# Performance work log

Hardware: AMD Instinct MI355X
Metric: run time of the kernel (lower is better)

## Reference

```python
import jax, jax.numpy as jnp
import numpy as np

G, K1, K2, N, NP, EPS = 16, 128, 32, 128, 512, 1e-5

def _bn(x, axes):
    m = jnp.mean(x, axes, keepdims=True)
    v = jnp.var(x, axes, keepdims=True)  # biased, as torch BN training mode
    return (x - m) * jax.lax.rsqrt(v + EPS)

def _fps(xyz, npoint):
    # farthest point sampling, deterministic start at index 0; xyz (B,P,3)
    B, P, _ = xyz.shape
    def step(carry, _):
        dists, far = carry
        c = jnp.take_along_axis(xyz, far[:, None, None], axis=1)   # (B,1,3)
        d = jnp.sum((xyz - c) ** 2, -1)                            # (B,P)
        dists = jnp.minimum(dists, d)
        return (dists, jnp.argmax(dists, -1)), far
    init = (jnp.full((B, P), 1e10, xyz.dtype), jnp.zeros((B,), jnp.int32))
    _, idx = jax.lax.scan(step, init, None, length=npoint)         # (npoint,B)
    return jnp.take_along_axis(xyz, idx.T[:, :, None], axis=1)     # (B,npoint,3)

def _pointnet(x, w1, b1, w2, b2, w3, b3):
    h = jax.nn.relu(_bn(x @ w1 + b1, (0, 1)))
    h = jax.nn.relu(_bn(h @ w2 + b2, (0, 1)))
    h = _bn(h @ w3 + b3, (0, 1))
    return jnp.max(h, axis=1)                                      # (B,1024)

def _mapping(feat, w1, b1, w2, b2, w3, b3, w4, b4):
    # all 16 branches stacked on leading axis g
    h = jax.nn.relu(_bn(jnp.einsum('bk,gkj->gbj', feat, w1) + b1[:, None, :], (1,)))
    h = jax.nn.relu(_bn(jnp.einsum('gbj,gjk->gbk', h, w2) + b2[:, None, :], (1,)))
    h = jax.nn.relu(_bn(jnp.einsum('gbj,gjk->gbk', h, w3) + b3[:, None, :], (1,)))
    return jax.nn.relu(_bn(jnp.einsum('gbj,gjk->gbk', h, w4) + b4[:, None, :], (1,)))

def _axform(feat, fw, fb, c1w, c1b, c2w, c2b, c3w, c3b, c4w, c4b):
    # feat (G,B,K1); 1x1 convs expressed as einsums in channels-last layout
    xb = (jnp.einsum('gbk,gkm->gbm', feat, fw) + fb[:, None, :]).reshape(G, -1, N, K2)
    h = jax.nn.relu(_bn(jnp.einsum('gbnk,gkc->gbnc', xb, c1w) + c1b[:, None, None, :], (1, 2)))
    h = jax.nn.relu(_bn(jnp.einsum('gbnc,gcd->gbnd', h, c2w) + c2b[:, None, None, :], (1, 2)))
    h = jnp.einsum('gbnd,gde->gbne', h, c3w) + c3b[:, None, None, :]  # (G,B,N,1024)
    w = jax.nn.softmax(h, axis=2)                                     # softmax over N
    y = jnp.einsum('gbne,gbnk->gbek', w, xb)                          # (G,B,1024,K2)
    return jnp.einsum('gbek,gkc->gbec', y, c4w) + c4b[:, None, None, :]  # (G,B,1024,3)

def _forward(x, pn, mp, gen, ref):
    x_partial = _fps(x, NP)                                           # (B,512,3)
    feat = _pointnet(x, *pn)                                          # (B,1024)
    mfeat = _mapping(feat, *mp)                                       # (G,B,K1)
    x1g = _axform(mfeat, *gen)                                        # (G,B,1024,3)
    B = x.shape[0]
    x_1 = jnp.transpose(x1g, (1, 0, 2, 3)).reshape(B, -1, 3)          # (B,16384,3)
    fps1 = jax.vmap(lambda p: _fps(p, NP))(x1g)                       # (G,B,512,3)
    x_base = jnp.concatenate([fps1, jnp.broadcast_to(x_partial, (G,) + x_partial.shape)], axis=2)
    x2g = x_base + _axform(mfeat, *ref)                               # (G,B,1024,3)
    x_2 = jnp.transpose(x2g, (1, 0, 2, 3)).reshape(B, -1, 3)
    return x_1, x_2

def setup_inputs() -> dict:
    keys = iter(jax.random.split(jax.random.key(0), 40))
    def rn(shape, s=0.02):
        return (s * jax.random.normal(next(keys), shape)).astype(jnp.float32)
    inp = {}
    inp['x'] = jax.random.normal(next(keys), (16, 2048, 3), jnp.float32)
    inp['pn_w1'] = rn((3, 64));      inp['pn_b1'] = rn((64,))
    inp['pn_w2'] = rn((64, 128));    inp['pn_b2'] = rn((128,))
    inp['pn_w3'] = rn((128, 1024));  inp['pn_b3'] = rn((1024,))
    inp['mp_w1'] = rn((G, 1024, 1024)); inp['mp_b1'] = rn((G, 1024))
    inp['mp_w2'] = rn((G, 1024, 1024)); inp['mp_b2'] = rn((G, 1024))
    inp['mp_w3'] = rn((G, 1024, 1024)); inp['mp_b3'] = rn((G, 1024))
    inp['mp_w4'] = rn((G, 1024, K1));   inp['mp_b4'] = rn((G, K1))
    for p in ('g', 'r'):
        inp[p + '_fw'] = rn((G, K1, N * K2)); inp[p + '_fb'] = rn((G, N * K2))
        inp[p + '_c1w'] = rn((G, K2, 64));    inp[p + '_c1b'] = rn((G, 64))
        inp[p + '_c2w'] = rn((G, 64, 128));   inp[p + '_c2b'] = rn((G, 128))
        inp[p + '_c3w'] = rn((G, 128, 1024)); inp[p + '_c3b'] = rn((G, 1024))
        inp[p + '_c4w'] = rn((G, K2, 3));     inp[p + '_c4b'] = rn((G, 3))
    return inp

def reference(x, pn_w1, pn_b1, pn_w2, pn_b2, pn_w3, pn_b3,
              mp_w1, mp_b1, mp_w2, mp_b2, mp_w3, mp_b3, mp_w4, mp_b4,
              g_fw, g_fb, g_c1w, g_c1b, g_c2w, g_c2b, g_c3w, g_c3b, g_c4w, g_c4b,
              r_fw, r_fb, r_c1w, r_c1b, r_c2w, r_c2b, r_c3w, r_c3b, r_c4w, r_c4b):
    pn = (pn_w1, pn_b1, pn_w2, pn_b2, pn_w3, pn_b3)
    mp = (mp_w1, mp_b1, mp_w2, mp_b2, mp_w3, mp_b3, mp_w4, mp_b4)
    gen = (g_fw, g_fb, g_c1w, g_c1b, g_c2w, g_c2b, g_c3w, g_c3b, g_c4w, g_c4b)
    ref = (r_fw, r_fb, r_c1w, r_c1b, r_c2w, r_c2b, r_c3w, r_c3b, r_c4w, r_c4b)
    return _forward(x, pn, mp, gen, ref)
```

## Files before the change

kernel.cpp:

```cpp
#include <hip/hip_runtime.h>
#include <math.h>

#define TID ((int)threadIdx.x)

namespace {
constexpr float EPSf = 1e-5f;

struct FpsArgs {
  const float* pts; float* out; float* dmin; int* far;
  int it0, it1, nc;
};

__device__ __forceinline__ unsigned fenc(float f){
  unsigned u = __float_as_uint(f);
  return (u & 0x80000000u) ? ~u : (u | 0x80000000u);
}
__device__ __forceinline__ float fdec(unsigned e){
  unsigned u = (e & 0x80000000u) ? (e & 0x7fffffffu) : ~e;
  return __uint_as_float(u);
}

template<int CTRL>
__device__ __forceinline__ void dpp_comb(float& bm, int& bp){
  int om_i = __builtin_amdgcn_update_dpp(__float_as_int(bm), __float_as_int(bm), CTRL, 0xf, 0xf, false);
  int op   = __builtin_amdgcn_update_dpp(bp, bp, CTRL, 0xf, 0xf, false);
  float om = __int_as_float(om_i);
  if (om > bm || (om == bm && op < bp)){ bm = om; bp = op; }
}

template<int LP, int NT>
__device__ void fps_body(const FpsArgs& a, int ci){
  const int NPTS = NT*LP;
  const float* pts = a.pts + (size_t)ci * NPTS * 3;
  float* out = a.out + (size_t)ci * 512 * 3;
  float* dst = a.dmin + (size_t)ci * NPTS;
  float px[LP], py[LP], pz[LP], dmin[LP];
#pragma unroll
  for (int j = 0; j < LP; j++){
    int p = TID + NT*j;
    px[j] = pts[p*3+0]; py[j] = pts[p*3+1]; pz[j] = pts[p*3+2];
  }
  int far;
  if (a.it0 == 0){
#pragma unroll
    for (int j = 0; j < LP; j++) dmin[j] = 1e10f;
    far = 0;
  } else {
#pragma unroll
    for (int j = 0; j < LP; j++) dmin[j] = dst[TID + NT*j];
    far = a.far[ci];
  }
  __shared__ unsigned long long red2[2][NT/64];
  for (int i = a.it0; i < a.it1; i++){
    float cx = pts[far*3+0], cy = pts[far*3+1], cz = pts[far*3+2];
    if (TID == 0){ out[i*3+0]=cx; out[i*3+1]=cy; out[i*3+2]=cz; }
    float bm = -1.f; int bp = 0;
#pragma unroll
    for (int j = 0; j < LP; j++){
      float dx = __fsub_rn(px[j], cx);
      float dy = __fsub_rn(py[j], cy);
      float dz = __fsub_rn(pz[j], cz);
      float d  = __fadd_rn(__fadd_rn(__fmul_rn(dx,dx), __fmul_rn(dy,dy)), __fmul_rn(dz,dz));
      float dm = fminf(dmin[j], d);
      dmin[j] = dm;
      if (dm > bm){ bm = dm; bp = TID + NT*j; }
    }
    dpp_comb<0x111>(bm,bp); dpp_comb<0x112>(bm,bp); dpp_comb<0x114>(bm,bp);
    dpp_comb<0x118>(bm,bp); dpp_comb<0x142>(bm,bp); dpp_comb<0x143>(bm,bp);
    unsigned long long key =
      ((unsigned long long)(unsigned)__builtin_amdgcn_readlane(__float_as_int(bm), 63) << 32)
      | (unsigned)~(unsigned)__builtin_amdgcn_readlane(bp, 63);
    if ((TID & 63) == 63) red2[i&1][TID>>6] = key;
    __syncthreads();
    unsigned long long kk = red2[i&1][0];
#pragma unroll
    for (int t = 1; t < NT/64; t++){
      unsigned long long o = red2[i&1][t];
      kk = kk > o ? kk : o;
    }
    far = (int)~(unsigned)kk;
  }
  if (a.it1 < 512){
#pragma unroll
    for (int j = 0; j < LP; j++) dst[TID + NT*j] = dmin[j];
    if (TID == 0) a.far[ci] = far;
  }
}

__device__ __forceinline__ int aswz64(int n, int k){
  return (n << 6) + ((((k >> 2) ^ ((n >> 3) & 3)) << 2) | (k & 3));
}
__device__ __forceinline__ int pswz(int n, int e){
  return (n << 6) + (e ^ (((n >> 3) & 3) << 3));
}

template<int C, int K, int FLP>
__global__ void __launch_bounds__(256) rowgemm_kernel(const float* __restrict__ in,
    const float* __restrict__ w, const float* __restrict__ bias, const float2* __restrict__ st2,
    float* __restrict__ out, int rows_per_g, FpsArgs fa)
{
  int bid = blockIdx.x;
  if constexpr (FLP > 0){
    if (bid < fa.nc){ fps_body<FLP,256>(fa, bid); return; }
    bid -= fa.nc;
  }
  constexpr int RPB = 256 / C;
  __shared__ float lin[RPB * K];
  size_t row0 = (size_t)bid * RPB;
  int g = (int)(row0 / rows_per_g);
  for (int i = TID; i < RPB*K; i += 256){
    float v = in[row0*(size_t)K + i];
    if (st2){ float2 s = st2[(size_t)g*K + (i % K)]; v = fmaxf((v - s.x)*s.y, 0.f); }
    lin[i] = v;
  }
  __syncthreads();
  int r = TID / C, c = TID % C;
  float acc = bias[(size_t)g*C + c];
  const float* wg = w + (size_t)g*K*C + c;
#pragma unroll
  for (int k = 0; k < K; k++) acc = fmaf(lin[r*K + k], wg[(size_t)k*C], acc);
  out[(row0 + r)*C + c] = acc;
}

template<int FLP>
__global__ void __launch_bounds__(256, 4) big1024b_kernel(const float* __restrict__ in,
    const float* __restrict__ w, const float* __restrict__ bias, const float2* __restrict__ st2,
    float* __restrict__ ps, float* __restrict__ pq, unsigned* __restrict__ maxenc, FpsArgs fa)
{
  int bid = blockIdx.x;
  if constexpr (FLP > 0){
    if (bid < fa.nc){ fps_body<FLP,256>(fa, bid); return; }
    bid -= fa.nc;
  }
  int rb = bid >> 1, ch = bid & 1;
  size_t row0 = (size_t)rb * 32;
  __shared__ float linT[4096];
  for (int i = TID; i < 4096; i += 256){
    int r = i >> 7, k = i & 127;
    float v = in[(row0 + r)*128 + k];
    float2 s = st2[k];
    linT[k*32 + r] = fmaxf((v - s.x)*s.y, 0.f);
  }
  __syncthreads();
  int rq = TID >> 6, cq = TID & 63;
  int c0 = ch*512 + cq*8;
  float acc[8][8];
  {
    float4 b0 = *(const float4*)(bias + c0);
    float4 b1 = *(const float4*)(bias + c0 + 4);
    const float bv[8] = {b0.x,b0.y,b0.z,b0.w,b1.x,b1.y,b1.z,b1.w};
#pragma unroll
    for (int ri = 0; ri < 8; ri++)
#pragma unroll
      for (int ci = 0; ci < 8; ci++) acc[ri][ci] = bv[ci];
  }
  const float* wp = w + c0;
#pragma unroll 2
  for (int k = 0; k < 128; k++){
    float4 w0 = *(const float4*)(wp + (size_t)k*1024);
    float4 w1 = *(const float4*)(wp + (size_t)k*1024 + 4);
    float4 l0 = *(const float4*)&linT[k*32 + rq*8];
    float4 l1 = *(const float4*)&linT[k*32 + rq*8 + 4];
    const float lv[8] = {l0.x,l0.y,l0.z,l0.w,l1.x,l1.y,l1.z,l1.w};
    const float wv[8] = {w0.x,w0.y,w0.z,w0.w,w1.x,w1.y,w1.z,w1.w};
#pragma unroll
    for (int ri = 0; ri < 8; ri++)
#pragma unroll
      for (int ci = 0; ci < 8; ci++)
        acc[ri][ci] = fmaf(lv[ri], wv[ci], acc[ri][ci]);
  }
  float s[8], q[8], m[8];
#pragma unroll
  for (int ci = 0; ci < 8; ci++){
    s[ci] = 0.f; q[ci] = 0.f; m[ci] = -1e38f;
#pragma unroll
    for (int ri = 0; ri < 8; ri++){
      float v = acc[ri][ci];
      s[ci] += v; q[ci] = fmaf(v, v, q[ci]); m[ci] = fmaxf(m[ci], v);
    }
  }
  __syncthreads();
  float* red = linT;
#pragma unroll
  for (int ci = 0; ci < 8; ci++){
    red[rq*512 + cq*8 + ci]        = s[ci];
    red[2048 + rq*512 + cq*8 + ci] = q[ci];
  }
  __syncthreads();
  if (rq == 0){
#pragma unroll
    for (int ci = 0; ci < 8; ci++){
      float ss = 0.f, qq = 0.f;
#pragma unroll
      for (int r = 0; r < 4; r++){
        ss += red[r*512 + cq*8 + ci];
        qq += red[2048 + r*512 + cq*8 + ci];
      }
      ps[(size_t)rb*1024 + c0 + ci] = ss;
      pq[(size_t)rb*1024 + c0 + ci] = qq;
    }
  }
  __syncthreads();
#pragma unroll
  for (int ci = 0; ci < 8; ci++) red[rq*512 + cq*8 + ci] = m[ci];
  __syncthreads();
  if (rq == 0){
    int b = (int)(row0 / 2048);
#pragma unroll
    for (int ci = 0; ci < 8; ci++){
      float mm = red[cq*8 + ci];
#pragma unroll
      for (int r = 1; r < 4; r++) mm = fmaxf(mm, red[r*512 + cq*8 + ci]);
      atomicMax(&maxenc[(size_t)b*1024 + c0 + ci], fenc(mm));
    }
  }
}

template<int FLP>
__global__ void __launch_bounds__(128) mapgemm2_kernel(const float* __restrict__ in, int in_gstride,
    const float* __restrict__ w, const float* __restrict__ bias, const float2* __restrict__ st2,
    float* __restrict__ out, int K, int J, int JB, int NS, FpsArgs fa)
{
  int bid = blockIdx.x;
  if constexpr (FLP > 0){
    if (bid < fa.nc){ fps_body<FLP,128>(fa, bid); return; }
    bid -= fa.nc;
  }
  int kc = bid / (JB*16);
  int g  = (bid / JB) % 16;
  int jb = bid % JB;
  int kchunk = K / NS, k0 = kc*kchunk;
  __shared__ float linT[128*16];
  const float* ing = in + (size_t)g * in_gstride;
  for (int i = TID; i < kchunk*16; i += 128){
    int b = i / kchunk, k = i - b*kchunk;
    float v = ing[(size_t)b*K + k0 + k];
    if (st2){ float2 s = st2[(size_t)g*K + k0 + k]; v = fmaxf((v - s.x)*s.y, 0.f); }
    linT[k*16 + b] = v;
  }
  __syncthreads();
  int bh = TID >> 6, jq = TID & 63;
  int j = jb*256 + jq*4;
  const float* wp = w + ((size_t)g*K + k0)*J + j;
  float4 a4[8];
#pragma unroll
  for (int bi = 0; bi < 8; bi++) a4[bi] = make_float4(0.f,0.f,0.f,0.f);
#pragma unroll 4
  for (int k = 0; k < kchunk; k++){
    float4 wv = *(const float4*)(wp + (size_t)k*J);
    float4 l0 = *(const float4*)&linT[k*16 + bh*8];
    float4 l1 = *(const float4*)&linT[k*16 + bh*8 + 4];
    const float lv[8] = {l0.x,l0.y,l0.z,l0.w,l1.x,l1.y,l1.z,l1.w};
#pragma unroll
    for (int bi = 0; bi < 8; bi++){
      a4[bi].x = fmaf(lv[bi], wv.x, a4[bi].x);
      a4[bi].y = fmaf(lv[bi], wv.y, a4[bi].y);
      a4[bi].z = fmaf(lv[bi], wv.z, a4[bi].z);
      a4[bi].w = fmaf(lv[bi], wv.w, a4[bi].w);
    }
  }
  if (NS == 1){
    float4 bv = *(const float4*)(bias + (size_t)g*J + j);
#pragma unroll
    for (int bi = 0; bi < 8; bi++){
      int b = bh*8 + bi;
      float4 o = make_float4(a4[bi].x+bv.x, a4[bi].y+bv.y, a4[bi].z+bv.z, a4[bi].w+bv.w);
      *(float4*)&out[((size_t)g*16 + b)*J + j] = o;
    }
  } else {
#pragma unroll
    for (int bi = 0; bi < 8; bi++)
      *(float4*)&out[(((size_t)kc*16 + g)*16 + bh*8 + bi)*J + j] = a4[bi];
  }
}

__global__ void __launch_bounds__(256) mapgemm_kernel(const float* __restrict__ in, int in_gstride,
    const float* __restrict__ w, const float* __restrict__ bias, const float2* __restrict__ st2,
    float* __restrict__ out, int K, int J, int JB, int NS)
{
  int bid = blockIdx.x;
  int kc = bid / (JB*16);
  int g  = (bid / JB) % 16;
  int jb = bid % JB;
  int j  = jb*256 + TID;
  bool jv = j < J;
  int jc = jv ? j : 0;
  int kchunk = K / NS;
  int k0 = kc * kchunk;
  __shared__ float lin[16 * 128];
  const float* ing = in + (size_t)g * in_gstride;
  float acc[16];
  float bv = (NS == 1 && jv) ? bias[(size_t)g*J + jc] : 0.f;
#pragma unroll
  for (int b = 0; b < 16; b++) acc[b] = bv;
  for (int kt = k0; kt < k0 + kchunk; kt += 128){
    __syncthreads();
    for (int i = TID; i < 2048; i += 256){
      int b = i >> 7, k = i & 127;
      float v = ing[(size_t)b*K + kt + k];
      if (st2){ float2 s = st2[(size_t)g*K + kt + k]; v = fmaxf((v - s.x)*s.y, 0.f); }
      lin[i] = v;
    }
    __syncthreads();
    const float* wg = w + ((size_t)g*K + kt)*J + jc;
    for (int k = 0; k < 128; k++){
      float wv = wg[(size_t)k*J];
#pragma unroll
      for (int b = 0; b < 16; b++) acc[b] = fmaf(lin[b*128 + k], wv, acc[b]);
    }
  }
  if (jv){
    if (NS == 1){
      for (int b = 0; b < 16; b++) out[((size_t)g*16 + b)*J + j] = acc[b];
    } else {
      for (int b = 0; b < 16; b++) out[(((size_t)kc*16 + g)*16 + b)*J + j] = acc[b];
    }
  }
}

__global__ void __launch_bounds__(256) redstats_kernel(const float* __restrict__ part,
    const float* __restrict__ bias, float* __restrict__ out, float2* __restrict__ st2,
    int J, int NS)
{
  int t = blockIdx.x*256 + TID;
  int g = t / J, j = t % J;
  float bv = bias[t];
  float s = 0.f, q = 0.f;
  for (int b = 0; b < 16; b++){
    float v = bv;
    for (int c = 0; c < NS; c++) v += part[(((size_t)c*16 + g)*16 + b)*J + j];
    out[((size_t)g*16 + b)*J + j] = v;
    s += v; q = fmaf(v, v, q);
  }
  float mean = s * (1.f/16.f);
  float var  = q * (1.f/16.f) - mean*mean;
  st2[t] = make_float2(mean, rsqrtf(fmaxf(var, 0.f) + EPSf));
}

__global__ void __launch_bounds__(256) statsacc_kernel(const float* __restrict__ in,
    float* __restrict__ part, int C, size_t chunk)
{
  size_t base = (size_t)blockIdx.x * chunk;
  int c = TID % C;
  float s = 0.f, q = 0.f;
  for (size_t idx = base + TID; idx < base + chunk; idx += 256){
    float v = in[idx]; s += v; q = fmaf(v, v, q);
  }
  __shared__ float ls[256], lq[256];
  ls[TID] = s; lq[TID] = q; __syncthreads();
  if (TID < C){
    for (int t = TID + C; t < 256; t += C){ s += ls[t]; q += lq[t]; }
    part[((size_t)blockIdx.x*C + c)*2]   = s;
    part[((size_t)blockIdx.x*C + c)*2+1] = q;
  }
}

__global__ void statsfin_kernel(const float* __restrict__ part, float2* __restrict__ st2,
    int C, int G, float invR)
{
  int slot = blockIdx.x*256 + TID;
  if (slot >= G*C) return;
  int g = slot / C, c = slot % C;
  int bpg = 256 / G;
  float s = 0.f, q = 0.f;
  for (int b = 0; b < bpg; b++){
    size_t p = ((size_t)(g*bpg + b)*C + c)*2;
    s += part[p]; q += part[p+1];
  }
  float mean = s*invR;
  float var  = q*invR - mean*mean;
  st2[slot] = make_float2(mean, rsqrtf(fmaxf(var, 0.f) + EPSf));
}

__global__ void pnfin_kernel(const float* __restrict__ ps, const float* __restrict__ pq,
                             float2* __restrict__ st)
{
  int c = blockIdx.x*256 + TID;
  float s = 0.f, q = 0.f;
  for (int rb = 0; rb < 1024; rb++){ s += ps[rb*1024 + c]; q += pq[rb*1024 + c]; }
  float mean = s * (1.f/32768.f);
  float var  = q * (1.f/32768.f) - mean*mean;
  st[c] = make_float2(mean, rsqrtf(fmaxf(var, 0.f) + EPSf));
}

__global__ void feat_kernel(const unsigned* __restrict__ me, const float2* __restrict__ st,
                            float* __restrict__ feat)
{
  int t = blockIdx.x*256 + TID;
  int c = t & 1023;
  float2 s = st[c];
  feat[t] = (fdec(me[t]) - s.x) * s.y;
}

template<int FLP>
__global__ void __launch_bounds__(256, 4) fused_kernel(const float* __restrict__ c2o,
    const float2* __restrict__ st2, const float* __restrict__ c3w,
    const float* __restrict__ xb, const float* __restrict__ c4w, const float* __restrict__ c4b,
    float* __restrict__ out_pts, float* __restrict__ out_x1, FpsArgs fa)
{
  int bid = blockIdx.x;
  if constexpr (FLP > 0){
    if (bid < fa.nc){ fps_body<FLP,256>(fa, bid); return; }
    bid -= fa.nc;
  }
  int gb = bid >> 3, eb = bid & 7;
  int g = gb >> 4, b = gb & 15;
  __shared__ float As[8192];
  __shared__ float xbl[4096];
  for (int i = TID; i < 4096; i += 256) xbl[i] = xb[(size_t)gb*4096 + i];

  int tn = TID >> 4, te = TID & 15;
  int n0 = tn*8, e0 = te*8;
  const float* wgp = c3w + ((size_t)g << 17) + eb*128 + e0;
  const float* src = c2o + (size_t)gb*16384;
  float h[8][8];
#pragma unroll
  for (int i = 0; i < 8; i++)
#pragma unroll
    for (int j = 0; j < 8; j++) h[i][j] = 0.f;

  for (int kh = 0; kh < 2; kh++){
    __syncthreads();
    for (int i = TID; i < 8192; i += 256){
      int n = i >> 6, k = i & 63;
      int kg = kh*64 + k;
      float2 s = st2[(size_t)g*128 + kg];
      As[aswz64(n,k)] = fmaxf((src[n*128 + kg] - s.x)*s.y, 0.f);
    }
    __syncthreads();
    for (int k4 = 0; k4 < 64; k4 += 4){
      float4 a[8];
#pragma unroll
      for (int i = 0; i < 8; i++) a[i] = *(const float4*)&As[aswz64(n0+i, k4)];
#pragma unroll
      for (int kk = 0; kk < 4; kk++){
        float4 wa = *(const float4*)(wgp + (size_t)(kh*64 + k4 + kk)*1024);
        float4 wb = *(const float4*)(wgp + (size_t)(kh*64 + k4 + kk)*1024 + 4);
#pragma unroll
        for (int i = 0; i < 8; i++){
          float av = (&a[i].x)[kk];
          h[i][0] = fmaf(av, wa.x, h[i][0]);
          h[i][1] = fmaf(av, wa.y, h[i][1]);
          h[i][2] = fmaf(av, wa.z, h[i][2]);
          h[i][3] = fmaf(av, wa.w, h[i][3]);
          h[i][4] = fmaf(av, wb.x, h[i][4]);
          h[i][5] = fmaf(av, wb.y, h[i][5]);
          h[i][6] = fmaf(av, wb.z, h[i][6]);
          h[i][7] = fmaf(av, wb.w, h[i][7]);
        }
      }
    }
  }

  for (int p = 0; p < 2; p++){
    __syncthreads();
    if ((te >> 3) == p){
      int el0 = (te & 7) * 8;
#pragma unroll
      for (int i = 0; i < 8; i++){
#pragma unroll
        for (int j4 = 0; j4 < 8; j4 += 4)
          *(float4*)&As[pswz(n0+i, el0+j4)] =
            make_float4(h[i][j4], h[i][j4+1], h[i][j4+2], h[i][j4+3]);
      }
    }
    __syncthreads();
    if (TID < 128){
      int el = TID >> 1, hh = TID & 1;
      float m = -1e38f;
      for (int jj = 0; jj < 64; jj++){
        int n = hh*64 + jj;
        m = fmaxf(m, As[pswz(n, el)]);
      }
      m = fmaxf(m, __shfl_xor(m, 1));
      float s = 0.f;
      float4 y[8];
#pragma unroll
      for (int q = 0; q < 8; q++) y[q] = make_float4(0.f,0.f,0.f,0.f);
      for (int jj = 0; jj < 64; jj++){
        int n = hh*64 + jj;
        float wv = __expf(As[pswz(n, el)] - m);
        s += wv;
        const float4* xr = (const float4*)&xbl[n*32];
#pragma unroll
        for (int q = 0; q < 8; q++){
          float4 xv = xr[q];
          y[q].x = fmaf(wv, xv.x, y[q].x);
          y[q].y = fmaf(wv, xv.y, y[q].y);
          y[q].z = fmaf(wv, xv.z, y[q].z);
          y[q].w = fmaf(wv, xv.w, y[q].w);
        }
      }
      s += __shfl_xor(s, 1);
#pragma unroll
      for (int q = 0; q < 8; q++){
        y[q].x += __shfl_xor(y[q].x, 1);
        y[q].y += __shfl_xor(y[q].y, 1);
        y[q].z += __shfl_xor(y[q].z, 1);
        y[q].w += __shfl_xor(y[q].w, 1);
      }
      if (hh == 0){
        const float* cw = c4w + g*96;
        float o0 = 0.f, o1 = 0.f, o2 = 0.f;
#pragma unroll
        for (int q = 0; q < 8; q++){
#pragma unroll
          for (int c2 = 0; c2 < 4; c2++){
            float yv = (&y[q].x)[c2];
            int k = q*4 + c2;
            o0 = fmaf(yv, cw[k*3+0], o0);
            o1 = fmaf(yv, cw[k*3+1], o1);
            o2 = fmaf(yv, cw[k*3+2], o2);
          }
        }
        float rs = 1.f / s;
        o0 = fmaf(rs, o0, c4b[g*3+0]);
        o1 = fmaf(rs, o1, c4b[g*3+1]);
        o2 = fmaf(rs, o2, c4b[g*3+2]);
        int eg = eb*128 + p*64 + el;
        size_t po = ((size_t)gb*1024 + eg)*3;
        out_pts[po+0] = o0; out_pts[po+1] = o1; out_pts[po+2] = o2;
        if (out_x1){
          size_t xo = (((size_t)b*16 + g)*1024 + eg)*3;
          out_x1[xo+0] = o0; out_x1[xo+1] = o1; out_x1[xo+2] = o2;
        }
      }
    }
  }
}

__global__ void combine_kernel(const float* __restrict__ fps1, const float* __restrict__ xpart,
                               const float* __restrict__ d2, float* __restrict__ x2)
{
  size_t i = (size_t)blockIdx.x*256 + TID;
  if (i >= (size_t)16*16*1024*3) return;
  int c = (int)(i % 3);
  size_t t = i / 3;
  int e = (int)(t % 1024);
  size_t gb = t / 1024;
  int g = (int)(gb >> 4), b = (int)(gb & 15);
  float base;
  if (e < 512) base = fps1[(gb*512 + e)*3 + c];
  else         base = xpart[((size_t)b*512 + (e - 512))*3 + c];
  x2[(((size_t)b*16384) + (size_t)g*1024 + e)*3 + c] = base + d2[i];
}

}

extern "C" void kernel_launch(void* const* d_in, const int* in_sizes, int n_in,
                              void* d_out, int out_size, void* d_ws, size_t ws_size,
                              hipStream_t stream)
{
  (void)in_sizes; (void)n_in; (void)out_size; (void)ws_size;
  const float* x    = (const float*)d_in[0];
  const float* pnw1 = (const float*)d_in[1];
  const float* pnb1 = (const float*)d_in[2];
  const float* pnw2 = (const float*)d_in[3];
  const float* pnb2 = (const float*)d_in[4];
  const float* pnw3 = (const float*)d_in[5];
  const float* pnb3 = (const float*)d_in[6];
  const float* mpw[4] = {(const float*)d_in[7],(const float*)d_in[9],(const float*)d_in[11],(const float*)d_in[13]};
  const float* mpb[4] = {(const float*)d_in[8],(const float*)d_in[10],(const float*)d_in[12],(const float*)d_in[14]};

  float* ws = (float*)d_ws;
  size_t o = 0;
  auto alloc = [&](size_t n){ float* p = ws + o; o += n; return p; };
  float* x_partial = alloc(24576);
  float* feat      = alloc(16384);
  float* mfeat     = alloc(32768);
  float2* st_pn1   = (float2*)alloc(128);
  float2* st_pn2   = (float2*)alloc(256);
  float2* st_pn3   = (float2*)alloc(2048);
  float2* st_c1    = (float2*)alloc(2048);
  float2* st_c2    = (float2*)alloc(4096);
  float2* st_map0  = (float2*)alloc(32768);
  float2* st_map1  = (float2*)alloc(32768);
  float2* st_map2  = (float2*)alloc(32768);
  float2* st_map3  = (float2*)alloc(4096);
  float* sa_part   = alloc(65536);
  float* pn_ps     = alloc(1048576);
  float* pn_pq     = alloc(1048576);
  unsigned* maxenc = (unsigned*)alloc(16384);
  float* mapA      = alloc(262144);
  float* mapB      = alloc(262144);
  float* mpart     = alloc(4194304);
  float* xb        = alloc(1048576);
  float* c1o       = alloc(2097152);
  float* c2o       = alloc(4194304);
  float* x1g       = alloc(786432);
  float* d2buf     = alloc(786432);
  float* fps1b     = alloc(393216);
  float* fpsA_dmin = alloc(32768);
  int*   fpsA_far  = (int*)alloc(16);
  float* fpsB_dmin = alloc(262144);
  int*   fpsB_far  = (int*)alloc(256);

  float* xout1 = (float*)d_out;
  float* xout2 = xout1 + 786432;

  hipMemsetAsync(maxenc, 0, 16384*sizeof(unsigned), stream);

  FpsArgs f0{};
  FpsArgs fa{x, x_partial, fpsA_dmin, fpsA_far, 0, 0, 16};

  fa.it0 = 0; fa.it1 = 64;
  rowgemm_kernel<64,3,8><<<8192+16, 256, 0, stream>>>(x, pnw1, pnb1, nullptr, c1o, 32768, fa);
  statsacc_kernel<<<256, 256, 0, stream>>>(c1o, sa_part, 64, 8192);
  statsfin_kernel<<<1, 256, 0, stream>>>(sa_part, st_pn1, 64, 1, 1.f/32768.f);
  fa.it0 = 64; fa.it1 = 128;
  rowgemm_kernel<128,64,8><<<16384+16, 256, 0, stream>>>(c1o, pnw2, pnb2, st_pn1, c2o, 32768, fa);
  statsacc_kernel<<<256, 256, 0, stream>>>(c2o, sa_part, 128, 16384);
  statsfin_kernel<<<1, 256, 0, stream>>>(sa_part, st_pn2, 128, 1, 1.f/32768.f);
  fa.it0 = 128; fa.it1 = 224;
  big1024b_kernel<8><<<2048+16, 256, 0, stream>>>(c2o, pnw3, pnb3, st_pn2,
                                                  pn_ps, pn_pq, maxenc, fa);
  pnfin_kernel<<<4, 256, 0, stream>>>(pn_ps, pn_pq, st_pn3);
  feat_kernel<<<64, 256, 0, stream>>>(maxenc, st_pn3, feat);

  fa.it0 = 224; fa.it1 = 288;
  mapgemm2_kernel<16><<<1024+16, 128, 0, stream>>>(feat, 0,     mpw[0], nullptr, nullptr, mpart, 1024, 1024, 4, 16, fa);
  redstats_kernel<<<64, 256, 0, stream>>>(mpart, mpb[0], mapA, st_map0, 1024, 16);
  fa.it0 = 288; fa.it1 = 352;
  mapgemm2_kernel<16><<<1024+16, 128, 0, stream>>>(mapA, 16384, mpw[1], nullptr, st_map0, mpart, 1024, 1024, 4, 16, fa);
  redstats_kernel<<<64, 256, 0, stream>>>(mpart, mpb[1], mapB, st_map1, 1024, 16);
  fa.it0 = 352; fa.it1 = 416;
  mapgemm2_kernel<16><<<1024+16, 128, 0, stream>>>(mapB, 16384, mpw[2], nullptr, st_map1, mpart, 1024, 1024, 4, 16, fa);
  redstats_kernel<<<64, 256, 0, stream>>>(mpart, mpb[2], mapA, st_map2, 1024, 16);
  mapgemm_kernel<<<64, 256, 0, stream>>>(mapA, 16384, mpw[3], nullptr, st_map2, mpart, 1024, 128, 1, 4);
  redstats_kernel<<<8, 256, 0, stream>>>(mpart, mpb[3], mfeat, st_map3, 128, 4);

  for (int p = 0; p < 2; p++){
    const float* fw  = (const float*)d_in[15 + p*10 + 0];
    const float* fb  = (const float*)d_in[15 + p*10 + 1];
    const float* c1w = (const float*)d_in[15 + p*10 + 2];
    const float* c1b = (const float*)d_in[15 + p*10 + 3];
    const float* c2w = (const float*)d_in[15 + p*10 + 4];
    const float* c2b = (const float*)d_in[15 + p*10 + 5];
    const float* c3w = (const float*)d_in[15 + p*10 + 6];
    const float* c4w = (const float*)d_in[15 + p*10 + 8];
    const float* c4b = (const float*)d_in[15 + p*10 + 9];

    if (p == 0){
      fa.it0 = 416; fa.it1 = 480;
      mapgemm2_kernel<16><<<256+16, 128, 0, stream>>>(mfeat, 2048, fw, fb, st_map3, xb, 128, 4096, 16, 1, fa);
      fa.it0 = 480; fa.it1 = 512;
      rowgemm_kernel<64,32,8><<<8192+16, 256, 0, stream>>>(xb, c1w, c1b, nullptr, c1o, 2048, fa);
      statsacc_kernel<<<256, 256, 0, stream>>>(c1o, sa_part, 64, 8192);
      statsfin_kernel<<<4, 256, 0, stream>>>(sa_part, st_c1, 64, 16, 1.f/2048.f);
      rowgemm_kernel<128,64,0><<<16384, 256, 0, stream>>>(c1o, c2w, c2b, st_c1, c2o, 2048, f0);
      statsacc_kernel<<<256, 256, 0, stream>>>(c2o, sa_part, 128, 16384);
      statsfin_kernel<<<8, 256, 0, stream>>>(sa_part, st_c2, 128, 16, 1.f/2048.f);
      fused_kernel<0><<<2048, 256, 0, stream>>>(c2o, st_c2, c3w, xb, c4w, c4b, x1g, xout1, f0);
    } else {
      FpsArgs fb_{x1g, fps1b, fpsB_dmin, fpsB_far, 0, 0, 256};
      mapgemm2_kernel<0><<<256, 128, 0, stream>>>(mfeat, 2048, fw, fb, st_map3, xb, 128, 4096, 16, 1, f0);
      fb_.it0 = 0; fb_.it1 = 64;
      rowgemm_kernel<64,32,4><<<8192+256, 256, 0, stream>>>(xb, c1w, c1b, nullptr, c1o, 2048, fb_);
      statsacc_kernel<<<256, 256, 0, stream>>>(c1o, sa_part, 64, 8192);
      statsfin_kernel<<<4, 256, 0, stream>>>(sa_part, st_c1, 64, 16, 1.f/2048.f);
      fb_.it0 = 64; fb_.it1 = 160;
      rowgemm_kernel<128,64,4><<<16384+256, 256, 0, stream>>>(c1o, c2w, c2b, st_c1, c2o, 2048, fb_);
      statsacc_kernel<<<256, 256, 0, stream>>>(c2o, sa_part, 128, 16384);
      statsfin_kernel<<<8, 256, 0, stream>>>(sa_part, st_c2, 128, 16, 1.f/2048.f);
      fb_.it0 = 160; fb_.it1 = 512;
      fused_kernel<4><<<2048+256, 256, 0, stream>>>(c2o, st_c2, c3w, xb, c4w, c4b, d2buf, nullptr, fb_);
    }
  }

  combine_kernel<<<3072, 256, 0, stream>>>(fps1b, x_partial, d2buf, xout2);
}
```

Measured before the change: 1.955 ms.

## Use bf16 MFMA for c3 GEMM in fused softmax kernel and redistribute FPS

Adds a weight-transpose kernel that converts the c3 weights to bf16 in an e-major layout. The fused kernel's 128x128x128 GEMM now runs on bf16 MFMA instructions instead of scalar FP32 FMAs, with swizzled LDS staging for both activations and weights. The softmax-weighted reduction is spread over all 256 threads instead of 128. FPS iterations for the second branch are also moved into the statsacc kernels to rebalance piggybacked work. The cost is bf16 rounding of the activations and weights before the softmax logits, which reduces precision.

Result: faster. 1.853 ms (-5.2%).

```diff
diff --git a/kernel.cpp b/kernel.cpp
--- a/kernel.cpp
+++ b/kernel.cpp
@@ -5,6 +5,9 @@
 
 namespace {
 constexpr float EPSf = 1e-5f;
+
+typedef __attribute__((ext_vector_type(8))) short short8;
+typedef __attribute__((ext_vector_type(4))) float f32x4;
 
 struct FpsArgs {
   const float* pts; float* out; float* dmin; int* far;
@@ -18,6 +21,10 @@
 __device__ __forceinline__ float fdec(unsigned e){
   unsigned u = (e & 0x80000000u) ? (e & 0x7fffffffu) : ~e;
   return __uint_as_float(u);
+}
+__device__ __forceinline__ short bf16rne(float f){
+  unsigned u = __float_as_uint(f);
+  return (short)((u + 0x7fffu + ((u >> 16) & 1u)) >> 16);
 }
 
 template<int CTRL>
@@ -87,11 +94,8 @@
   }
 }
 
-__device__ __forceinline__ int aswz64(int n, int k){
-  return (n << 6) + ((((k >> 2) ^ ((n >> 3) & 3)) << 2) | (k & 3));
-}
 __device__ __forceinline__ int pswz(int n, int e){
-  return (n << 6) + (e ^ (((n >> 3) & 3) << 3));
+  return (n << 6) + (e ^ (((n >> 3) & 3) << 3) ^ ((n >> 5) & 3));
 }
 
 template<int C, int K, int FLP>
@@ -337,10 +341,16 @@
   st2[t] = make_float2(mean, rsqrtf(fmaxf(var, 0.f) + EPSf));
 }
 
+template<int FLP>
 __global__ void __launch_bounds__(256) statsacc_kernel(const float* __restrict__ in,
-    float* __restrict__ part, int C, size_t chunk)
-{
-  size_t base = (size_t)blockIdx.x * chunk;
+    float* __restrict__ part, int C, size_t chunk, FpsArgs fa)
+{
+  int bid = blockIdx.x;
+  if constexpr (FLP > 0){
+    if (bid < fa.nc){ fps_body<FLP,256>(fa, bid); return; }
+    bid -= fa.nc;
+  }
+  size_t base = (size_t)bid * chunk;
   int c = TID % C;
   float s = 0.f, q = 0.f;
   for (size_t idx = base + TID; idx < base + chunk; idx += 256){
@@ -350,8 +360,8 @@
   ls[TID] = s; lq[TID] = q; __syncthreads();
   if (TID < C){
     for (int t = TID + C; t < 256; t += C){ s += ls[t]; q += lq[t]; }
-    part[((size_t)blockIdx.x*C + c)*2]   = s;
-    part[((size_t)blockIdx.x*C + c)*2+1] = q;
+    part[((size_t)bid*C + c)*2]   = s;
+    part[((size_t)bid*C + c)*2+1] = q;
   }
 }
 
@@ -392,9 +402,25 @@
   feat[t] = (fdec(me[t]) - s.x) * s.y;
 }
 
+__global__ void __launch_bounds__(256) wtr_kernel(const float* __restrict__ c3w,
+                                                  short* __restrict__ wt)
+{
+  int g = blockIdx.x >> 4, kt = blockIdx.x & 15;
+  __shared__ float lds[8*1024];
+  const float* src = c3w + ((size_t)g*128 + kt*8)*1024;
+  for (int i = TID; i < 8192; i += 256) lds[i] = src[i];
+  __syncthreads();
+  for (int e = TID; e < 1024; e += 256){
+    short8 v;
+#pragma unroll
+    for (int j = 0; j < 8; j++) v[j] = bf16rne(lds[j*1024 + e]);
+    *(short8*)&wt[((size_t)g*1024 + e)*128 + kt*8] = v;
+  }
+}
+
 template<int FLP>
 __global__ void __launch_bounds__(256, 4) fused_kernel(const float* __restrict__ c2o,
-    const float2* __restrict__ st2, const float* __restrict__ c3w,
+    const float2* __restrict__ st2, const short* __restrict__ wt,
     const float* __restrict__ xb, const float* __restrict__ c4w, const float* __restrict__ c4b,
     float* __restrict__ out_pts, float* __restrict__ out_x1, FpsArgs fa)
 {
@@ -405,125 +431,127 @@
   }
   int gb = bid >> 3, eb = bid & 7;
   int g = gb >> 4, b = gb & 15;
-  __shared__ float As[8192];
+  __shared__ short Abf[16384];
   __shared__ float xbl[4096];
-  for (int i = TID; i < 4096; i += 256) xbl[i] = xb[(size_t)gb*4096 + i];
-
-  int tn = TID >> 4, te = TID & 15;
-  int n0 = tn*8, e0 = te*8;
-  const float* wgp = c3w + ((size_t)g << 17) + eb*128 + e0;
+  float* Ps = (float*)Abf;
+
+  for (int i = TID; i < 1024; i += 256){
+    int n = i >> 3, q = i & 7;
+    float4 v = *(const float4*)(xb + (size_t)gb*4096 + n*32 + q*4);
+    *(float4*)&xbl[n*32 + ((q ^ ((n>>5)&3))<<2)] = v;
+  }
   const float* src = c2o + (size_t)gb*16384;
-  float h[8][8];
-#pragma unroll
-  for (int i = 0; i < 8; i++)
-#pragma unroll
-    for (int j = 0; j < 8; j++) h[i][j] = 0.f;
-
-  for (int kh = 0; kh < 2; kh++){
-    __syncthreads();
-    for (int i = TID; i < 8192; i += 256){
-      int n = i >> 6, k = i & 63;
-      int kg = kh*64 + k;
-      float2 s = st2[(size_t)g*128 + kg];
-      As[aswz64(n,k)] = fmaxf((src[n*128 + kg] - s.x)*s.y, 0.f);
-    }
-    __syncthreads();
-    for (int k4 = 0; k4 < 64; k4 += 4){
-      float4 a[8];
-#pragma unroll
-      for (int i = 0; i < 8; i++) a[i] = *(const float4*)&As[aswz64(n0+i, k4)];
-#pragma unroll
-      for (int kk = 0; kk < 4; kk++){
-        float4 wa = *(const float4*)(wgp + (size_t)(kh*64 + k4 + kk)*1024);
-        float4 wb = *(const float4*)(wgp + (size_t)(kh*64 + k4 + kk)*1024 + 4);
-#pragma unroll
-        for (int i = 0; i < 8; i++){
-          float av = (&a[i].x)[kk];
-          h[i][0] = fmaf(av, wa.x, h[i][0]);
-          h[i][1] = fmaf(av, wa.y, h[i][1]);
-          h[i][2] = fmaf(av, wa.z, h[i][2]);
-          h[i][3] = fmaf(av, wa.w, h[i][3]);
-          h[i][4] = fmaf(av, wb.x, h[i][4]);
-          h[i][5] = fmaf(av, wb.y, h[i][5]);
-          h[i][6] = fmaf(av, wb.z, h[i][6]);
-          h[i][7] = fmaf(av, wb.w, h[i][7]);
+  for (int i = TID; i < 2048; i += 256){
+    int n = i >> 4, kc = i & 15;
+    float4 a0 = *(const float4*)(src + n*128 + kc*8);
+    float4 a1 = *(const float4*)(src + n*128 + kc*8 + 4);
+    const float vals[8] = {a0.x,a0.y,a0.z,a0.w,a1.x,a1.y,a1.z,a1.w};
+    short8 ob;
+#pragma unroll
+    for (int j = 0; j < 8; j++){
+      float2 s = st2[(size_t)g*128 + kc*8 + j];
+      ob[j] = bf16rne(fmaxf((vals[j] - s.x)*s.y, 0.f));
+    }
+    *(short8*)&Abf[n*128 + ((kc ^ (n & 7)) << 3)] = ob;
+  }
+  __syncthreads();
+
+  int lane = TID & 63, wid = TID >> 6;
+  int lr = lane & 15, lkg = lane >> 4;
+  f32x4 acc[2][8];
+#pragma unroll
+  for (int nt = 0; nt < 2; nt++)
+#pragma unroll
+    for (int et = 0; et < 8; et++) acc[nt][et] = (f32x4){0.f,0.f,0.f,0.f};
+
+  const short* wtg = wt + ((size_t)g*1024 + eb*128)*128;
+#pragma unroll
+  for (int kt = 0; kt < 4; kt++){
+    int kb = kt*32 + lkg*8;
+    int kcf = kb >> 3;
+    short8 afr[2];
+#pragma unroll
+    for (int nt = 0; nt < 2; nt++){
+      int row = wid*32 + nt*16 + lr;
+      afr[nt] = *(const short8*)&Abf[row*128 + ((kcf ^ (row & 7)) << 3)];
+    }
+#pragma unroll
+    for (int et = 0; et < 8; et++){
+      short8 bfr = *(const short8*)&wtg[(et*16 + lr)*128 + kb];
+      acc[0][et] = __builtin_amdgcn_mfma_f32_16x16x32_bf16(afr[0], bfr, acc[0][et], 0, 0, 0);
+      acc[1][et] = __builtin_amdgcn_mfma_f32_16x16x32_bf16(afr[1], bfr, acc[1][et], 0, 0, 0);
+    }
+  }
+  __syncthreads();
+
+  for (int p = 0; p < 2; p++){
+    if (p) __syncthreads();
+#pragma unroll
+    for (int nt = 0; nt < 2; nt++)
+#pragma unroll
+      for (int t = 0; t < 4; t++){
+        int et = p*4 + t;
+#pragma unroll
+        for (int r = 0; r < 4; r++){
+          int n = wid*32 + nt*16 + lkg*4 + r;
+          Ps[pswz(n, t*16 + lr)] = acc[nt][et][r];
         }
       }
-    }
-  }
-
-  for (int p = 0; p < 2; p++){
     __syncthreads();
-    if ((te >> 3) == p){
-      int el0 = (te & 7) * 8;
-#pragma unroll
-      for (int i = 0; i < 8; i++){
-#pragma unroll
-        for (int j4 = 0; j4 < 8; j4 += 4)
-          *(float4*)&As[pswz(n0+i, el0+j4)] =
-            make_float4(h[i][j4], h[i][j4+1], h[i][j4+2], h[i][j4+3]);
+    int el = TID >> 2, hq = TID & 3;
+    float m = -1e38f;
+    for (int j = 0; j < 32; j++) m = fmaxf(m, Ps[pswz(hq*32 + j, el)]);
+    m = fmaxf(m, __shfl_xor(m, 1));
+    m = fmaxf(m, __shfl_xor(m, 2));
+    float s = 0.f;
+    float4 y[8];
+#pragma unroll
+    for (int q = 0; q < 8; q++) y[q] = make_float4(0.f,0.f,0.f,0.f);
+    for (int j = 0; j < 32; j++){
+      int n = hq*32 + j;
+      float wv = __expf(Ps[pswz(n, el)] - m);
+      s += wv;
+#pragma unroll
+      for (int q = 0; q < 8; q++){
+        float4 xv = *(const float4*)&xbl[n*32 + ((q ^ hq) << 2)];
+        y[q].x = fmaf(wv, xv.x, y[q].x);
+        y[q].y = fmaf(wv, xv.y, y[q].y);
+        y[q].z = fmaf(wv, xv.z, y[q].z);
+        y[q].w = fmaf(wv, xv.w, y[q].w);
       }
     }
-    __syncthreads();
-    if (TID < 128){
-      int el = TID >> 1, hh = TID & 1;
-      float m = -1e38f;
-      for (int jj = 0; jj < 64; jj++){
-        int n = hh*64 + jj;
-        m = fmaxf(m, As[pswz(n, el)]);
-      }
-      m = fmaxf(m, __shfl_xor(m, 1));
-      float s = 0.f;
-      float4 y[8];
-#pragma unroll
-      for (int q = 0; q < 8; q++) y[q] = make_float4(0.f,0.f,0.f,0.f);
-      for (int jj = 0; jj < 64; jj++){
-        int n = hh*64 + jj;
-        float wv = __expf(As[pswz(n, el)] - m);
-        s += wv;
-        const float4* xr = (const float4*)&xbl[n*32];
-#pragma unroll
-        for (int q = 0; q < 8; q++){
-          float4 xv = xr[q];
-          y[q].x = fmaf(wv, xv.x, y[q].x);
-          y[q].y = fmaf(wv, xv.y, y[q].y);
-          y[q].z = fmaf(wv, xv.z, y[q].z);
-          y[q].w = fmaf(wv, xv.w, y[q].w);
+    s += __shfl_xor(s, 1); s += __shfl_xor(s, 2);
+#pragma unroll
+    for (int q = 0; q < 8; q++){
+      y[q].x += __shfl_xor(y[q].x, 1); y[q].x += __shfl_xor(y[q].x, 2);
+      y[q].y += __shfl_xor(y[q].y, 1); y[q].y += __shfl_xor(y[q].y, 2);
+      y[q].z += __shfl_xor(y[q].z, 1); y[q].z += __shfl_xor(y[q].z, 2);
+      y[q].w += __shfl_xor(y[q].w, 1); y[q].w += __shfl_xor(y[q].w, 2);
+    }
+    if (hq == 0){
+      const float* cw = c4w + g*96;
+      float o0 = 0.f, o1 = 0.f, o2 = 0.f;
+#pragma unroll
+      for (int q = 0; q < 8; q++){
+#pragma unroll
+        for (int c2 = 0; c2 < 4; c2++){
+          float yv = (&y[q].x)[c2];
+          int k = q*4 + c2;
+          o0 = fmaf(yv, cw[k*3+0], o0);
+          o1 = fmaf(yv, cw[k*3+1], o1);
+          o2 = fmaf(yv, cw[k*3+2], o2);
         }
       }
-      s += __shfl_xor(s, 1);
-#pragma unroll
-      for (int q = 0; q < 8; q++){
-        y[q].x += __shfl_xor(y[q].x, 1);
-        y[q].y += __shfl_xor(y[q].y, 1);
-        y[q].z += __shfl_xor(y[q].z, 1);
-        y[q].w += __shfl_xor(y[q].w, 1);
-      }
-      if (hh == 0){
-        const float* cw = c4w + g*96;
-        float o0 = 0.f, o1 = 0.f, o2 = 0.f;
-#pragma unroll
-        for (int q = 0; q < 8; q++){
-#pragma unroll
-          for (int c2 = 0; c2 < 4; c2++){
-            float yv = (&y[q].x)[c2];
-            int k = q*4 + c2;
-            o0 = fmaf(yv, cw[k*3+0], o0);
-            o1 = fmaf(yv, cw[k*3+1], o1);
-            o2 = fmaf(yv, cw[k*3+2], o2);
-          }
-        }
-        float rs = 1.f / s;
-        o0 = fmaf(rs, o0, c4b[g*3+0]);
-        o1 = fmaf(rs, o1, c4b[g*3+1]);
-        o2 = fmaf(rs, o2, c4b[g*3+2]);
-        int eg = eb*128 + p*64 + el;
-        size_t po = ((size_t)gb*1024 + eg)*3;
-        out_pts[po+0] = o0; out_pts[po+1] = o1; out_pts[po+2] = o2;
-        if (out_x1){
-          size_t xo = (((size_t)b*16 + g)*1024 + eg)*3;
-          out_x1[xo+0] = o0; out_x1[xo+1] = o1; out_x1[xo+2] = o2;
-        }
+      float rs = 1.f / s;
+      o0 = fmaf(rs, o0, c4b[g*3+0]);
+      o1 = fmaf(rs, o1, c4b[g*3+1]);
+      o2 = fmaf(rs, o2, c4b[g*3+2]);
+      int eg = eb*128 + p*64 + el;
+      size_t po = ((size_t)gb*1024 + eg)*3;
+      out_pts[po+0] = o0; out_pts[po+1] = o1; out_pts[po+2] = o2;
+      if (out_x1){
+        size_t xo = (((size_t)b*16 + g)*1024 + eg)*3;
+        out_x1[xo+0] = o0; out_x1[xo+1] = o1; out_x1[xo+2] = o2;
       }
     }
   }
@@ -594,22 +622,27 @@
   int*   fpsA_far  = (int*)alloc(16);
   float* fpsB_dmin = alloc(262144);
   int*   fpsB_far  = (int*)alloc(256);
+  short* wt_g      = (short*)alloc(1048576);
+  short* wt_r      = (short*)alloc(1048576);
 
   float* xout1 = (float*)d_out;
   float* xout2 = xout1 + 786432;
 
   hipMemsetAsync(maxenc, 0, 16384*sizeof(unsigned), stream);
 
+  wtr_kernel<<<256, 256, 0, stream>>>((const float*)d_in[21], wt_g);
+  wtr_kernel<<<256, 256, 0, stream>>>((const float*)d_in[31], wt_r);
+
   FpsArgs f0{};
   FpsArgs fa{x, x_partial, fpsA_dmin, fpsA_far, 0, 0, 16};
 
   fa.it0 = 0; fa.it1 = 64;
   rowgemm_kernel<64,3,8><<<8192+16, 256, 0, stream>>>(x, pnw1, pnb1, nullptr, c1o, 32768, fa);
-  statsacc_kernel<<<256, 256, 0, stream>>>(c1o, sa_part, 64, 8192);
+  statsacc_kernel<0><<<256, 256, 0, stream>>>(c1o, sa_part, 64, 8192, f0);
   statsfin_kernel<<<1, 256, 0, stream>>>(sa_part, st_pn1, 64, 1, 1.f/32768.f);
   fa.it0 = 64; fa.it1 = 128;
   rowgemm_kernel<128,64,8><<<16384+16, 256, 0, stream>>>(c1o, pnw2, pnb2, st_pn1, c2o, 32768, fa);
-  statsacc_kernel<<<256, 256, 0, stream>>>(c2o, sa_part, 128, 16384);
+  statsacc_kernel<0><<<256, 256, 0, stream>>>(c2o, sa_part, 128, 16384, f0);
   statsfin_kernel<<<1, 256, 0, stream>>>(sa_part, st_pn2, 128, 1, 1.f/32768.f);
   fa.it0 = 128; fa.it1 = 224;
   big1024b_kernel<8><<<2048+16, 256, 0, stream>>>(c2o, pnw3, pnb3, st_pn2,
@@ -636,7 +669,6 @@
     const float* c1b = (const float*)d_in[15 + p*10 + 3];
     const float* c2w = (const float*)d_in[15 + p*10 + 4];
     const float* c2b = (const float*)d_in[15 + p*10 + 5];
-    const float* c3w = (const float*)d_in[15 + p*10 + 6];
     const float* c4w = (const float*)d_in[15 + p*10 + 8];
     const float* c4b = (const float*)d_in[15 + p*10 + 9];
 
@@ -645,25 +677,27 @@
       mapgemm2_kernel<16><<<256+16, 128, 0, stream>>>(mfeat, 2048, fw, fb, st_map3, xb, 128, 4096, 16, 1, fa);
       fa.it0 = 480; fa.it1 = 512;
       rowgemm_kernel<64,32,8><<<8192+16, 256, 0, stream>>>(xb, c1w, c1b, nullptr, c1o, 2048, fa);
-      statsacc_kernel<<<256, 256, 0, stream>>>(c1o, sa_part, 64, 8192);
+      statsacc_kernel<0><<<256, 256, 0, stream>>>(c1o, sa_part, 64, 8192, f0);
       statsfin_kernel<<<4, 256, 0, stream>>>(sa_part, st_c1, 64, 16, 1.f/2048.f);
       rowgemm_kernel<128,64,0><<<16384, 256, 0, stream>>>(c1o, c2w, c2b, st_c1, c2o, 2048, f0);
-      statsacc_kernel<<<256, 256, 0, stream>>>(c2o, sa_part, 128, 16384);
+      statsacc_kernel<0><<<256, 256, 0, stream>>>(c2o, sa_part, 128, 16384, f0);
       statsfin_kernel<<<8, 256, 0, stream>>>(sa_part, st_c2, 128, 16, 1.f/2048.f);
-      fused_kernel<0><<<2048, 256, 0, stream>>>(c2o, st_c2, c3w, xb, c4w, c4b, x1g, xout1, f0);
+      fused_kernel<0><<<2048, 256, 0, stream>>>(c2o, st_c2, wt_g, xb, c4w, c4b, x1g, xout1, f0);
     } else {
       FpsArgs fb_{x1g, fps1b, fpsB_dmin, fpsB_far, 0, 0, 256};
       mapgemm2_kernel<0><<<256, 128, 0, stream>>>(mfeat, 2048, fw, fb, st_map3, xb, 128, 4096, 16, 1, f0);
-      fb_.it0 = 0; fb_.it1 = 64;
+      fb_.it0 = 0; fb_.it1 = 72;
       rowgemm_kernel<64,32,4><<<8192+256, 256, 0, stream>>>(xb, c1w, c1b, nullptr, c1o, 2048, fb_);
-      statsacc_kernel<<<256, 256, 0, stream>>>(c1o, sa_part, 64, 8192);
+      fb_.it0 = 72; fb_.it1 = 104;
+      statsacc_kernel<4><<<256+256, 256, 0, stream>>>(c1o, sa_part, 64, 8192, fb_);
       statsfin_kernel<<<4, 256, 0, stream>>>(sa_part, st_c1, 64, 16, 1.f/2048.f);
-      fb_.it0 = 64; fb_.it1 = 160;
+      fb_.it0 = 104; fb_.it1 = 208;
       rowgemm_kernel<128,64,4><<<16384+256, 256, 0, stream>>>(c1o, c2w, c2b, st_c1, c2o, 2048, fb_);
-      statsacc_kernel<<<256, 256, 0, stream>>>(c2o, sa_part, 128, 16384);
+      fb_.it0 = 208; fb_.it1 = 240;
+      statsacc_kernel<4><<<256+256, 256, 0, stream>>>(c2o, sa_part, 128, 16384, fb_);
       statsfin_kernel<<<8, 256, 0, stream>>>(sa_part, st_c2, 128, 16, 1.f/2048.f);
-      fb_.it0 = 160; fb_.it1 = 512;
-      fused_kernel<4><<<2048+256, 256, 0, stream>>>(c2o, st_c2, c3w, xb, c4w, c4b, d2buf, nullptr, fb_);
+      fb_.it0 = 240; fb_.it1 = 512;
+      fused_kernel<4><<<2048+256, 256, 0, stream>>>(c2o, st_c2, wt_r, xb, c4w, c4b, d2buf, nullptr, fb_);
     }
   }
 
```
